# Optimization experiments

Hardware: AMD Instinct MI355X
Metric: run time of the kernel (lower is better)

Reference implementation:

```python
import jax, jax.numpy as jnp
import numpy as np

EMB = 1024
FF = 4 * EMB

def _ternary(w):
    # BitNet b1.58 absmean quantization; forward uses pure ternary weights
    scale = jnp.maximum(jnp.mean(jnp.abs(w)), 1e-8)
    w_t = jnp.clip(jnp.round(w / scale), -1.0, 1.0)
    # STE: forward = w_t, backward = identity w.r.t. w
    return w + jax.lax.stop_gradient(w_t - w)

def setup_inputs() -> dict:
    key = jax.random.key(0)
    kx, k1, k2, kb1, kb2 = jax.random.split(key, 5)
    x = jax.random.normal(kx, (4, 2048, EMB), dtype=jnp.float32)
    # nn.Linear default init: U(-1/sqrt(fan_in), 1/sqrt(fan_in))
    lim1 = 1.0 / np.sqrt(EMB)
    lim2 = 1.0 / np.sqrt(FF)
    W1 = jax.random.uniform(k1, (FF, EMB), jnp.float32, -lim1, lim1)
    b1 = jax.random.uniform(kb1, (FF,), jnp.float32, -lim1, lim1)
    W2 = jax.random.uniform(k2, (EMB, FF), jnp.float32, -lim2, lim2)
    b2 = jax.random.uniform(kb2, (EMB,), jnp.float32, -lim2, lim2)
    return {"x": x, "W1": W1, "b1": b1, "W2": W2, "b2": b2}

def reference(x, W1, b1, W2, b2):
    h = jnp.einsum('bsd,fd->bsf', x, _ternary(W1)) + b1  # [B,S,FF]
    h = jax.nn.gelu(h, approximate=False)  # torch nn.GELU default = exact erf
    out = jnp.einsum('bsf,df->bsd', h, _ternary(W2)) + b2  # [B,S,EMB]
    return out
```

## Files before the change

kernel.cpp:

```cpp
#include <hip/hip_runtime.h>
#include <hip/hip_bf16.h>
#include <cstdint>
#include <cstddef>

typedef __bf16 bf16x8 __attribute__((ext_vector_type(8)));
typedef float  f32x4  __attribute__((ext_vector_type(4)));

__device__ __forceinline__ unsigned short f2bf(float f) {
    __hip_bfloat16 b = __float2bfloat16(f);
    return *reinterpret_cast<unsigned short*>(&b);
}

__device__ __forceinline__ float fast_gelu(float x) {
    float x2 = x * x;
    float m  = x * __builtin_fmaf(x2, -0.10294314f, -2.30220795f);
    float e  = __builtin_amdgcn_exp2f(m);
    return x * __builtin_amdgcn_rcpf(1.0f + e);
}


__global__ void zero2_kernel(float* p) {
    if (threadIdx.x < 2) p[threadIdx.x] = 0.0f;
}

__global__ void abs_sum2_kernel(const float4* __restrict__ w0, const float4* __restrict__ w1,
                                int n4, float* __restrict__ out) {
    int half = (int)blockIdx.x >> 9;
    const float4* w = half ? w1 : w0;
    int b = (int)blockIdx.x & 511;
    float s = 0.0f;
    for (int i = b * blockDim.x + threadIdx.x; i < n4; i += 512 * blockDim.x) {
        float4 v = w[i];
        s += fabsf(v.x) + fabsf(v.y) + fabsf(v.z) + fabsf(v.w);
    }
    #pragma unroll
    for (int o = 32; o > 0; o >>= 1) s += __shfl_down(s, o, 64);
    __shared__ float part[4];
    int lane = threadIdx.x & 63, wid = threadIdx.x >> 6;
    if (lane == 0) part[wid] = s;
    __syncthreads();
    if (threadIdx.x == 0) atomicAdd(&out[half], part[0] + part[1] + part[2] + part[3]);
}

__global__ void prep_kernel(const float4* __restrict__ w0, ushort4* __restrict__ t0,
                            const float4* __restrict__ w1, ushort4* __restrict__ t1,
                            int n4w,
                            const float4* __restrict__ x, ushort4* __restrict__ xb,
                            int n4x,
                            const float* __restrict__ sum, float inv_n) {
    int seg = (int)blockIdx.x >> 10;
    int b = (int)blockIdx.x & 1023;
    if (seg == 2) {
        for (int i = b * blockDim.x + threadIdx.x; i < n4x; i += 1024 * blockDim.x) {
            float4 v = x[i];
            ushort4 o;
            o.x = f2bf(v.x); o.y = f2bf(v.y); o.z = f2bf(v.z); o.w = f2bf(v.w);
            xb[i] = o;
        }
        return;
    }
    const float4* w = seg ? w1 : w0;
    ushort4* t = seg ? t1 : t0;
    float scale = fmaxf(sum[seg] * inv_n, 1e-8f);
    float inv = 1.0f / scale;
    for (int i = b * blockDim.x + threadIdx.x; i < n4w; i += 1024 * blockDim.x) {
        float4 v = w[i];
        ushort4 o;
        o.x = f2bf(fminf(fmaxf(rintf(v.x * inv), -1.0f), 1.0f));
        o.y = f2bf(fminf(fmaxf(rintf(v.y * inv), -1.0f), 1.0f));
        o.z = f2bf(fminf(fmaxf(rintf(v.z * inv), -1.0f), 1.0f));
        o.w = f2bf(fminf(fmaxf(rintf(v.w * inv), -1.0f), 1.0f));
        t[i] = o;
    }
}


template <int EPI, int K, int N>
__global__ __launch_bounds__(256)
void gemm_bt_kernel(const unsigned short* __restrict__ A,
                    const unsigned short* __restrict__ B,
                    const float* __restrict__ bias,
                    void* __restrict__ C) {
    __shared__ __align__(16) unsigned short As[128 * 64];
    __shared__ __align__(16) unsigned short Bs[128 * 64];

    const int tid  = threadIdx.x;
    const int lane = tid & 63;
    const int wid  = tid >> 6;
    const int wr   = wid >> 1;
    const int wc   = wid & 1;
    const int mBase = wr * 64;
    const int nBase = wc * 64;
    const int lr = lane & 15;
    const int lq = lane >> 4;

    const size_t aRow0 = (size_t)blockIdx.y * 128;
    const size_t bRow0 = (size_t)blockIdx.x * 128;

    const int rA  = tid >> 3;
    const int cSw = (((tid & 7) ^ (rA & 7)) << 3);
    const unsigned short* ga = A + (aRow0 + rA) * (size_t)K + cSw;
    const unsigned short* gb = B + (bRow0 + rA) * (size_t)K + cSw;
    unsigned short* ldsA = &As[tid * 8];
    unsigned short* ldsB = &Bs[tid * 8];

    f32x4 acc[4][4];
    #pragma unroll
    for (int i = 0; i < 4; ++i)
        #pragma unroll
        for (int j = 0; j < 4; ++j)
            acc[i][j] = f32x4{0.f, 0.f, 0.f, 0.f};

    const int swz0 = ((lq ^ (lr & 7)) << 3);
    const int swz1 = (((4 + lq) ^ (lr & 7)) << 3);

    #pragma unroll 2
    for (int k0 = 0; k0 < K; k0 += 64) {
        __syncthreads();
        #pragma unroll
        for (int t = 0; t < 4; ++t) {
            __builtin_amdgcn_global_load_lds(
                (const __attribute__((address_space(1))) void*)(ga + (size_t)t * 32 * K),
                (__attribute__((address_space(3))) void*)(ldsA + t * 2048), 16, 0, 0);
            __builtin_amdgcn_global_load_lds(
                (const __attribute__((address_space(1))) void*)(gb + (size_t)t * 32 * K),
                (__attribute__((address_space(3))) void*)(ldsB + t * 2048), 16, 0, 0);
        }
        ga += 64;
        gb += 64;
        __syncthreads();
        #pragma unroll
        for (int ks = 0; ks < 2; ++ks) {
            const int swz = ks ? swz1 : swz0;
            bf16x8 avec[4], bvec[4];
            #pragma unroll
            for (int i = 0; i < 4; ++i) {
                avec[i] = *(const bf16x8*)&As[(mBase + i * 16 + lr) * 64 + swz];
                bvec[i] = *(const bf16x8*)&Bs[(nBase + i * 16 + lr) * 64 + swz];
            }
            #pragma unroll
            for (int mi = 0; mi < 4; ++mi)
                #pragma unroll
                for (int ni = 0; ni < 4; ++ni)
                    acc[mi][ni] = __builtin_amdgcn_mfma_f32_16x16x32_bf16(
                        avec[mi], bvec[ni], acc[mi][ni], 0, 0, 0);
        }
    }

    #pragma unroll
    for (int mi = 0; mi < 4; ++mi) {
        #pragma unroll
        for (int ni = 0; ni < 4; ++ni) {
            int col = (int)bRow0 + nBase + ni * 16 + lr;
            float bv = bias[col];
            #pragma unroll
            for (int r = 0; r < 4; ++r) {
                size_t row = aRow0 + mBase + mi * 16 + lq * 4 + r;
                float v = acc[mi][ni][r] + bv;
                if (EPI == 0) {
                    ((unsigned short*)C)[row * (size_t)N + col] = f2bf(fast_gelu(v));
                } else {
                    ((float*)C)[row * (size_t)N + col] = v;
                }
            }
        }
    }
}


extern "C" void kernel_launch(void* const* d_in, const int* in_sizes, int n_in,
                              void* d_out, int out_size, void* d_ws, size_t ws_size,
                              hipStream_t stream) {
    const float* x  = (const float*)d_in[0];
    const float* W1 = (const float*)d_in[1];
    const float* b1 = (const float*)d_in[2];
    const float* W2 = (const float*)d_in[3];
    const float* b2 = (const float*)d_in[4];
    float* out = (float*)d_out;

    const int M = 8192, EMB = 1024, FF = 4096;
    const int nW = FF * EMB;

    char* ws = (char*)d_ws;
    float* sums = (float*)ws;
    unsigned short* W1t = (unsigned short*)(ws + 256);
    unsigned short* W2t = W1t + (size_t)nW;
    unsigned short* xb  = W2t + (size_t)nW;
    unsigned short* h   = xb  + (size_t)M * EMB;

    zero2_kernel<<<1, 64, 0, stream>>>(sums);
    abs_sum2_kernel<<<1024, 256, 0, stream>>>((const float4*)W1, (const float4*)W2,
                                              nW / 4, sums);
    prep_kernel<<<3072, 256, 0, stream>>>((const float4*)W1, (ushort4*)W1t,
                                          (const float4*)W2, (ushort4*)W2t, nW / 4,
                                          (const float4*)x, (ushort4*)xb, (M * EMB) / 4,
                                          sums, 1.0f / nW);

    gemm_bt_kernel<0, 1024, 4096><<<dim3(FF / 128, M / 128), 256, 0, stream>>>(xb, W1t, b1, h);
    gemm_bt_kernel<1, 4096, 1024><<<dim3(EMB / 128, M / 128), 256, 0, stream>>>(h, W2t, b2, out);
}
```

Before: 279.9 us.

## Fuse x bf16 conversion into first GEMM and drop atomic abs-sum

Removes the separate pass that converts x to bf16. The first GEMM now loads fp32 x tiles directly, converts them in registers and stores them swizzled into LDS. The weight abs-sum now writes per-block partials that each ternarize block reduces itself, which eliminates the zeroing kernel and the atomics. The trade-off is that the A-tile load in GEMM1 becomes a synchronous register path with extra conversion work and doubled fp32 read bytes, instead of an async direct-to-LDS copy.

```diff
diff --git a/kernel.cpp b/kernel.cpp
--- a/kernel.cpp
+++ b/kernel.cpp
@@ -5,6 +5,7 @@
 
 typedef __bf16 bf16x8 __attribute__((ext_vector_type(8)));
 typedef float  f32x4  __attribute__((ext_vector_type(4)));
+typedef unsigned short us8 __attribute__((ext_vector_type(8)));
 
 __device__ __forceinline__ unsigned short f2bf(float f) {
     __hip_bfloat16 b = __float2bfloat16(f);
@@ -19,12 +20,8 @@
 }
 
 
-__global__ void zero2_kernel(float* p) {
-    if (threadIdx.x < 2) p[threadIdx.x] = 0.0f;
-}
-
 __global__ void abs_sum2_kernel(const float4* __restrict__ w0, const float4* __restrict__ w1,
-                                int n4, float* __restrict__ out) {
+                                int n4, float* __restrict__ part) {
     int half = (int)blockIdx.x >> 9;
     const float4* w = half ? w1 : w0;
     int b = (int)blockIdx.x & 511;
@@ -35,34 +32,37 @@
     }
     #pragma unroll
     for (int o = 32; o > 0; o >>= 1) s += __shfl_down(s, o, 64);
-    __shared__ float part[4];
+    __shared__ float ps[4];
     int lane = threadIdx.x & 63, wid = threadIdx.x >> 6;
-    if (lane == 0) part[wid] = s;
+    if (lane == 0) ps[wid] = s;
     __syncthreads();
-    if (threadIdx.x == 0) atomicAdd(&out[half], part[0] + part[1] + part[2] + part[3]);
-}
-
-__global__ void prep_kernel(const float4* __restrict__ w0, ushort4* __restrict__ t0,
-                            const float4* __restrict__ w1, ushort4* __restrict__ t1,
-                            int n4w,
-                            const float4* __restrict__ x, ushort4* __restrict__ xb,
-                            int n4x,
-                            const float* __restrict__ sum, float inv_n) {
+    if (threadIdx.x == 0) part[blockIdx.x] = ps[0] + ps[1] + ps[2] + ps[3];
+}
+
+__global__ void ternarize_kernel(const float4* __restrict__ w0, ushort4* __restrict__ t0,
+                                 const float4* __restrict__ w1, ushort4* __restrict__ t1,
+                                 int n4w, const float* __restrict__ part, float inv_n) {
     int seg = (int)blockIdx.x >> 10;
     int b = (int)blockIdx.x & 1023;
-    if (seg == 2) {
-        for (int i = b * blockDim.x + threadIdx.x; i < n4x; i += 1024 * blockDim.x) {
-            float4 v = x[i];
-            ushort4 o;
-            o.x = f2bf(v.x); o.y = f2bf(v.y); o.z = f2bf(v.z); o.w = f2bf(v.w);
-            xb[i] = o;
-        }
-        return;
-    }
+
+    float s = 0.0f;
+    for (int j = threadIdx.x; j < 512; j += 256) s += part[seg * 512 + j];
+    #pragma unroll
+    for (int o = 32; o > 0; o >>= 1) s += __shfl_down(s, o, 64);
+    __shared__ float ps[4];
+    __shared__ float sscale;
+    int lane = threadIdx.x & 63, wid = threadIdx.x >> 6;
+    if (lane == 0) ps[wid] = s;
+    __syncthreads();
+    if (threadIdx.x == 0) {
+        float tot = ps[0] + ps[1] + ps[2] + ps[3];
+        sscale = fmaxf(tot * inv_n, 1e-8f);
+    }
+    __syncthreads();
+    float inv = 1.0f / sscale;
+
     const float4* w = seg ? w1 : w0;
     ushort4* t = seg ? t1 : t0;
-    float scale = fmaxf(sum[seg] * inv_n, 1e-8f);
-    float inv = 1.0f / scale;
     for (int i = b * blockDim.x + threadIdx.x; i < n4w; i += 1024 * blockDim.x) {
         float4 v = w[i];
         ushort4 o;
@@ -75,22 +75,117 @@
 }
 
 
-template <int EPI, int K, int N>
+template <int K, int N>
 __global__ __launch_bounds__(256)
-void gemm_bt_kernel(const unsigned short* __restrict__ A,
-                    const unsigned short* __restrict__ B,
-                    const float* __restrict__ bias,
-                    void* __restrict__ C) {
+void gemm1_kernel(const float* __restrict__ X,
+                  const unsigned short* __restrict__ B,
+                  const float* __restrict__ bias,
+                  unsigned short* __restrict__ C) {
     __shared__ __align__(16) unsigned short As[128 * 64];
     __shared__ __align__(16) unsigned short Bs[128 * 64];
 
     const int tid  = threadIdx.x;
     const int lane = tid & 63;
     const int wid  = tid >> 6;
-    const int wr   = wid >> 1;
-    const int wc   = wid & 1;
-    const int mBase = wr * 64;
-    const int nBase = wc * 64;
+    const int mBase = (wid >> 1) * 64;
+    const int nBase = (wid & 1) * 64;
+    const int lr = lane & 15;
+    const int lq = lane >> 4;
+
+    const size_t aRow0 = (size_t)blockIdx.y * 128;
+    const size_t bRow0 = (size_t)blockIdx.x * 128;
+
+    const int rA = tid >> 3;
+    const int cA = tid & 7;
+    const int pA = cA ^ (rA & 7);
+    const float* gx = X + (aRow0 + rA) * (size_t)K + cA * 8;
+    const unsigned short* gb = B + (bRow0 + rA) * (size_t)K + pA * 8;
+    unsigned short* ldsAw = &As[rA * 64 + pA * 8];
+    unsigned short* ldsB  = &Bs[tid * 8];
+
+    f32x4 acc[4][4];
+    #pragma unroll
+    for (int i = 0; i < 4; ++i)
+        #pragma unroll
+        for (int j = 0; j < 4; ++j)
+            acc[i][j] = f32x4{0.f, 0.f, 0.f, 0.f};
+
+    const int swz0 = ((lq ^ (lr & 7)) << 3);
+    const int swz1 = (((4 + lq) ^ (lr & 7)) << 3);
+
+    for (int k0 = 0; k0 < K; k0 += 64) {
+        __syncthreads();
+        #pragma unroll
+        for (int t = 0; t < 4; ++t)
+            __builtin_amdgcn_global_load_lds(
+                (const __attribute__((address_space(1))) void*)(gb + (size_t)t * 32 * K),
+                (__attribute__((address_space(3))) void*)(ldsB + t * 2048), 16, 0, 0);
+        gb += 64;
+        f32x4 lo[4], hi[4];
+        #pragma unroll
+        for (int t = 0; t < 4; ++t) {
+            lo[t] = *(const f32x4*)(gx + (size_t)t * 32 * K);
+            hi[t] = *(const f32x4*)(gx + (size_t)t * 32 * K + 4);
+        }
+        gx += 64;
+        #pragma unroll
+        for (int t = 0; t < 4; ++t) {
+            us8 v;
+            v[0] = f2bf(lo[t][0]); v[1] = f2bf(lo[t][1]);
+            v[2] = f2bf(lo[t][2]); v[3] = f2bf(lo[t][3]);
+            v[4] = f2bf(hi[t][0]); v[5] = f2bf(hi[t][1]);
+            v[6] = f2bf(hi[t][2]); v[7] = f2bf(hi[t][3]);
+            *(us8*)(ldsAw + t * 2048) = v;
+        }
+        __syncthreads();
+        #pragma unroll
+        for (int ks = 0; ks < 2; ++ks) {
+            const int swz = ks ? swz1 : swz0;
+            bf16x8 avec[4], bvec[4];
+            #pragma unroll
+            for (int i = 0; i < 4; ++i) {
+                avec[i] = *(const bf16x8*)&As[(mBase + i * 16 + lr) * 64 + swz];
+                bvec[i] = *(const bf16x8*)&Bs[(nBase + i * 16 + lr) * 64 + swz];
+            }
+            #pragma unroll
+            for (int mi = 0; mi < 4; ++mi)
+                #pragma unroll
+                for (int ni = 0; ni < 4; ++ni)
+                    acc[mi][ni] = __builtin_amdgcn_mfma_f32_16x16x32_bf16(
+                        avec[mi], bvec[ni], acc[mi][ni], 0, 0, 0);
+        }
+    }
+
+    #pragma unroll
+    for (int mi = 0; mi < 4; ++mi) {
+        #pragma unroll
+        for (int ni = 0; ni < 4; ++ni) {
+            int col = (int)bRow0 + nBase + ni * 16 + lr;
+            float bv = bias[col];
+            #pragma unroll
+            for (int r = 0; r < 4; ++r) {
+                size_t row = aRow0 + mBase + mi * 16 + lq * 4 + r;
+                C[row * (size_t)N + col] = f2bf(fast_gelu(acc[mi][ni][r] + bv));
+            }
+        }
+    }
+}
+
+
+template <int K, int N>
+__global__ __launch_bounds__(256)
+void gemm2_kernel(const unsigned short* __restrict__ A,
+                  const unsigned short* __restrict__ B,
+                  const float* __restrict__ bias,
+                  float* __restrict__ C) {
+    __shared__ __align__(16) unsigned short As[128 * 64];
+    __shared__ __align__(16) unsigned short Bs[128 * 64];
+
+    const int tid  = threadIdx.x;
+    const int lane = tid & 63;
+    const int wid  = tid >> 6;
+    const int mBase = (wid >> 1) * 64;
+    const int nBase = (wid & 1) * 64;
     const int lr = lane & 15;
     const int lq = lane >> 4;
 
@@ -156,12 +251,7 @@
             #pragma unroll
             for (int r = 0; r < 4; ++r) {
                 size_t row = aRow0 + mBase + mi * 16 + lq * 4 + r;
-                float v = acc[mi][ni][r] + bv;
-                if (EPI == 0) {
-                    ((unsigned short*)C)[row * (size_t)N + col] = f2bf(fast_gelu(v));
-                } else {
-                    ((float*)C)[row * (size_t)N + col] = v;
-                }
+                C[row * (size_t)N + col] = acc[mi][ni][r] + bv;
             }
         }
     }
@@ -182,20 +272,17 @@
     const int nW = FF * EMB;
 
     char* ws = (char*)d_ws;
-    float* sums = (float*)ws;
-    unsigned short* W1t = (unsigned short*)(ws + 256);
+    float* part = (float*)ws;
+    unsigned short* W1t = (unsigned short*)(ws + 16384);
     unsigned short* W2t = W1t + (size_t)nW;
-    unsigned short* xb  = W2t + (size_t)nW;
-    unsigned short* h   = xb  + (size_t)M * EMB;
-
-    zero2_kernel<<<1, 64, 0, stream>>>(sums);
+    unsigned short* h   = W2t + (size_t)nW;
+
     abs_sum2_kernel<<<1024, 256, 0, stream>>>((const float4*)W1, (const float4*)W2,
-                                              nW / 4, sums);
-    prep_kernel<<<3072, 256, 0, stream>>>((const float4*)W1, (ushort4*)W1t,
-                                          (const float4*)W2, (ushort4*)W2t, nW / 4,
-                                          (const float4*)x, (ushort4*)xb, (M * EMB) / 4,
-                                          sums, 1.0f / nW);
-
-    gemm_bt_kernel<0, 1024, 4096><<<dim3(FF / 128, M / 128), 256, 0, stream>>>(xb, W1t, b1, h);
-    gemm_bt_kernel<1, 4096, 1024><<<dim3(EMB / 128, M / 128), 256, 0, stream>>>(h, W2t, b2, out);
-}
+                                              nW / 4, part);
+    ternarize_kernel<<<2048, 256, 0, stream>>>((const float4*)W1, (ushort4*)W1t,
+                                               (const float4*)W2, (ushort4*)W2t,
+                                               nW / 4, part, 1.0f / nW);
+
+    gemm1_kernel<1024, 4096><<<dim3(FF / 128, M / 128), 256, 0, stream>>>(x, W1t, b1, h);
+    gemm2_kernel<4096, 1024><<<dim3(EMB / 128, M / 128), 256, 0, stream>>>(h, W2t, b2, out);
+}
```

After: 315.7 us. +12.8%, slower.
